# Kernel optimization log

Measured on AMD Instinct MI355X. Metric: run time of the kernel, lower is better.

## Reference

```python
import jax, jax.numpy as jnp
import numpy as np

N_VERTS = 40962   # icosphere level-6 vertices
N_POOL = 10242    # icosphere level-5 vertices (post-pool)
K = 7             # 6 neighbors + self
C1, C2, C3 = 64, 64, 128
IN_CH, OUT_CH = 8, 64
BATCH = 8


def setup_inputs() -> dict:
    key = jax.random.key(0)
    ks = jax.random.split(key, 10)
    x = jax.random.normal(ks[0], (BATCH, IN_CH, N_VERTS), dtype=jnp.float32)
    # neighbor order: 6 random neighbors + self at every 7th slot (as in my_get_neighs_order)
    neb6 = jax.random.randint(ks[1], (N_VERTS, 6), 0, N_VERTS)
    nebs = jnp.concatenate([neb6, jnp.arange(N_VERTS)[:, None]], axis=1).reshape(-1).astype(jnp.int64)
    s1 = 1.0 / np.sqrt(IN_CH)
    s2 = 1.0 / np.sqrt(C1 * K)
    s3 = 1.0 / np.sqrt(C2)
    sf = 1.0 / np.sqrt(C3 * N_POOL)
    W1 = jax.random.uniform(ks[2], (C1, IN_CH), jnp.float32, -s1, s1)
    b1 = jax.random.uniform(ks[3], (C1,), jnp.float32, -s1, s1)
    W2 = jax.random.uniform(ks[4], (C2, C1, K), jnp.float32, -s2, s2)
    b2 = jax.random.uniform(ks[5], (C2,), jnp.float32, -s2, s2)
    W3 = jax.random.uniform(ks[6], (C3, C2), jnp.float32, -s3, s3)
    b3 = jax.random.uniform(ks[7], (C3,), jnp.float32, -s3, s3)
    Wfc = jax.random.uniform(ks[8], (OUT_CH, C3 * N_POOL), jnp.float32, -sf, sf)
    bfc = jax.random.uniform(ks[9], (OUT_CH,), jnp.float32, -sf, sf)
    return {"x": x, "nebs": nebs, "W1": W1, "b1": b1, "W2": W2, "b2": b2,
            "W3": W3, "b3": b3, "Wfc": Wfc, "bfc": bfc}


def reference(x, nebs, W1, b1, W2, b2, W3, b3, Wfc, bfc):
    B = x.shape[0]
    # conv1: 1x1 conv == pointwise matmul over channels
    h1 = jax.nn.relu(jnp.einsum('bci,oc->boi', x, W1) + b1[None, :, None])  # [B,64,N]
    # gather neighbor features, then stride-7 conv collapses the 7 neighbor slots
    g1 = h1[:, :, nebs].reshape(B, C1, N_VERTS, K)                           # [B,64,N,7]
    h2 = jax.nn.relu(jnp.einsum('bcnk,ock->bon', g1, W2) + b2[None, :, None])  # [B,64,N]
    # gather for the first 10242 vertices, maxpool over the 7 neighbor slots
    g2 = h2[:, :, nebs[:N_POOL * K]].reshape(B, C2, N_POOL, K)
    p = jnp.max(g2, axis=-1)                                                  # [B,64,10242]
    # conv3: 1x1 conv
    h3 = jax.nn.relu(jnp.einsum('bci,oc->boi', p, W3) + b3[None, :, None])   # [B,128,10242]
    # dropout is identity in eval mode
    flat = h3.reshape(B, -1)                                                  # [B, 128*10242]
    return flat @ Wfc.T + bfc                                                 # [B, out_ch]
```

## Files before the change

### kernel.cpp

```cpp
#include <hip/hip_runtime.h>

#define NV 40962
#define NP 10242
#define KNB 7
#define C1 64
#define C2 64
#define C3 128
#define INC 8
#define OC 64
#define B 8
#define FCK (C3*NP)
#define NCHUNK (FCK/128)
#define FBLK 1024

typedef __attribute__((ext_vector_type(8))) __bf16 bf16x8;
typedef __attribute__((ext_vector_type(4))) float f32x4;
typedef unsigned short ushort_t;
typedef unsigned int uint_t;

static __device__ __forceinline__ ushort_t f2bf(float f) {
    uint_t u = __float_as_uint(f);
    u = (u + 0x7FFFu + ((u >> 16) & 1u)) >> 16;
    return (ushort_t)u;
}
static __device__ __forceinline__ uint_t pack2(float a, float b) {
    return (uint_t)f2bf(a) | ((uint_t)f2bf(b) << 16);
}

__global__ __launch_bounds__(256) void k_wswz(const float* __restrict__ W2,
        const float* __restrict__ W3, ushort_t* __restrict__ wsw) {
    int idx = blockIdx.x*256 + threadIdx.x;
    if (idx < 28672) {
        int j = idx & 7, lane = (idx >> 3) & 63, rest = idx >> 9;
        int ntile = rest & 3, kstep = rest >> 2;
        int quad = lane >> 4, col = lane & 15;
        int k = kstep*32 + quad*8 + j;
        int o = ntile*16 + col;
        int c = k & 63, knb = k >> 6;
        wsw[idx] = f2bf(W2[(size_t)o*(C1*KNB) + c*KNB + knb]);
    } else if (idx < 28672 + 8192) {
        int s = idx - 28672;
        int j = s & 7, lane = (s >> 3) & 63, rest = s >> 9;
        int ntile = rest & 7, kstep = rest >> 3;
        int quad = lane >> 4, col = lane & 15;
        int c = kstep*32 + quad*8 + j;
        int o3 = ntile*16 + col;
        wsw[idx] = f2bf(W3[(size_t)o3*C2 + c]);
    }
}

__global__ __launch_bounds__(256) void k_conv1(const float* __restrict__ x,
        const float* __restrict__ W1, const float* __restrict__ b1,
        ushort_t* __restrict__ h1bf) {
    __shared__ float sW[C1*INC];
    __shared__ float sb[C1];
    int tid = threadIdx.x;
    for (int i = tid; i < C1*INC; i += 256) sW[i] = W1[i];
    if (tid < C1) sb[tid] = b1[tid];
    __syncthreads();
    long g = (long)blockIdx.x*256 + tid;
    if (g >= (long)NV*B) return;
    int n = (int)(g >> 3);
    int b = (int)(g & 7);
    float xv[INC];
#pragma unroll
    for (int c = 0; c < INC; ++c) xv[c] = x[(size_t)b*INC*NV + (size_t)c*NV + n];
    uint4* outp = (uint4*)(h1bf + ((size_t)n*B + b)*C1);
#pragma unroll
    for (int og = 0; og < 8; ++og) {
        float h[8];
#pragma unroll
        for (int j = 0; j < 8; ++j) {
            int o = og*8 + j;
            float a = sb[o];
#pragma unroll
            for (int c = 0; c < INC; ++c) a += xv[c]*sW[o*INC + c];
            h[j] = fmaxf(a, 0.f);
        }
        uint4 u;
        u.x = pack2(h[0], h[1]); u.y = pack2(h[2], h[3]);
        u.z = pack2(h[4], h[5]); u.w = pack2(h[6], h[7]);
        outp[og] = u;
    }
}

__global__ __launch_bounds__(256) void k_conv2m(const ushort_t* __restrict__ h1bf,
        const int* __restrict__ nebs, const ushort_t* __restrict__ wsw,
        const float* __restrict__ b2, ushort_t* __restrict__ h2bf) {
    int tid = threadIdx.x;
    int wave = tid >> 6, lane = tid & 63;
    int quad = lane >> 4, col = lane & 15;
    int bsub = col & 7;
    int mblock = blockIdx.x * 128;
    int mbase[2];
    int rowt[2][KNB];
    f32x4 acc[2][4];
#pragma unroll
    for (int t = 0; t < 2; ++t) {
        mbase[t] = mblock + wave*32 + t*16;
        int v = (mbase[t] + col) >> 3;
        int vc = v < NV ? v : 0;
#pragma unroll
        for (int kn = 0; kn < KNB; ++kn) rowt[t][kn] = nebs[(size_t)vc*KNB + kn];
#pragma unroll
        for (int nt = 0; nt < 4; ++nt) acc[t][nt] = (f32x4){0.f, 0.f, 0.f, 0.f};
    }
    float bv[4];
#pragma unroll
    for (int nt = 0; nt < 4; ++nt) bv[nt] = b2[nt*16 + col];
    const bf16x8* W = (const bf16x8*)wsw;
#pragma unroll
    for (int ks = 0; ks < 14; ++ks) {
        int knb = ks >> 1;
        int c0 = (ks & 1)*32 + quad*8;
        bf16x8 a0 = *(const bf16x8*)(h1bf + ((size_t)rowt[0][knb]*B + bsub)*C1 + c0);
        bf16x8 a1 = *(const bf16x8*)(h1bf + ((size_t)rowt[1][knb]*B + bsub)*C1 + c0);
#pragma unroll
        for (int nt = 0; nt < 4; ++nt) {
            bf16x8 bf = W[(ks*4 + nt)*64 + lane];
            acc[0][nt] = __builtin_amdgcn_mfma_f32_16x16x32_bf16(a0, bf, acc[0][nt], 0, 0, 0);
            acc[1][nt] = __builtin_amdgcn_mfma_f32_16x16x32_bf16(a1, bf, acc[1][nt], 0, 0, 0);
        }
    }
#pragma unroll
    for (int t = 0; t < 2; ++t) {
#pragma unroll
        for (int r = 0; r < 4; ++r) {
            int m = mbase[t] + quad*4 + r;
            if ((m >> 3) < NV) {
#pragma unroll
                for (int nt = 0; nt < 4; ++nt) {
                    float val = fmaxf(acc[t][nt][r] + bv[nt], 0.f);
                    h2bf[(size_t)m*C2 + nt*16 + col] = f2bf(val);
                }
            }
        }
    }
}

__global__ __launch_bounds__(256) void k_pool(const ushort_t* __restrict__ h2bf,
        const int* __restrict__ nebs, ushort_t* __restrict__ pbf) {
    long t = (long)blockIdx.x*256 + threadIdx.x;
    if (t >= (long)NP*32) return;
    int cg = (int)(t & 3);
    int b  = (int)((t >> 2) & 7);
    int v  = (int)(t >> 5);
    float m[16];
#pragma unroll
    for (int i = 0; i < 16; ++i) m[i] = -1e30f;
    for (int kn = 0; kn < KNB; ++kn) {
        int row = nebs[(size_t)v*KNB + kn];
        const uint4* src = (const uint4*)(h2bf + ((size_t)row*B + b)*C2 + cg*16);
        uint4 u0 = src[0], u1 = src[1];
        uint_t ws[8] = {u0.x, u0.y, u0.z, u0.w, u1.x, u1.y, u1.z, u1.w};
#pragma unroll
        for (int i = 0; i < 8; ++i) {
            float lo = __uint_as_float((ws[i] & 0xFFFFu) << 16);
            float hi = __uint_as_float(ws[i] & 0xFFFF0000u);
            m[2*i]   = fmaxf(m[2*i], lo);
            m[2*i+1] = fmaxf(m[2*i+1], hi);
        }
    }
    uint_t op[8];
#pragma unroll
    for (int i = 0; i < 8; ++i) {
        uint_t lo = __float_as_uint(m[2*i]) >> 16;
        uint_t hi = __float_as_uint(m[2*i+1]) & 0xFFFF0000u;
        op[i] = lo | hi;
    }
    uint4* dst = (uint4*)(pbf + ((size_t)v*B + b)*C2 + cg*16);
    dst[0] = make_uint4(op[0], op[1], op[2], op[3]);
    dst[1] = make_uint4(op[4], op[5], op[6], op[7]);
}

__global__ __launch_bounds__(256) void k_conv3m(const ushort_t* __restrict__ pbf,
        const ushort_t* __restrict__ wsw3, const float* __restrict__ b3,
        float* __restrict__ h3) {
    int tid = threadIdx.x;
    int wave = tid >> 6, lane = tid & 63;
    int quad = lane >> 4, col = lane & 15;
    int m0 = blockIdx.x*64 + wave*16;
    int m = m0 + col;
    int mc = ((m >> 3) < NP) ? m : 0;
    f32x4 acc[8];
#pragma unroll
    for (int nt = 0; nt < 8; ++nt) acc[nt] = (f32x4){0.f, 0.f, 0.f, 0.f};
    float bv[8];
#pragma unroll
    for (int nt = 0; nt < 8; ++nt) bv[nt] = b3[nt*16 + col];
    const bf16x8* W = (const bf16x8*)wsw3;
#pragma unroll
    for (int ks = 0; ks < 2; ++ks) {
        bf16x8 a = *(const bf16x8*)(pbf + (size_t)mc*C2 + ks*32 + quad*8);
#pragma unroll
        for (int nt = 0; nt < 8; ++nt) {
            bf16x8 bf = W[(ks*8 + nt)*64 + lane];
            acc[nt] = __builtin_amdgcn_mfma_f32_16x16x32_bf16(a, bf, acc[nt], 0, 0, 0);
        }
    }
#pragma unroll
    for (int r = 0; r < 4; ++r) {
        int mm = m0 + quad*4 + r;
        int v = mm >> 3, b = mm & 7;
        if (v < NP) {
#pragma unroll
            for (int nt = 0; nt < 8; ++nt) {
                int o3 = nt*16 + col;
                h3[(size_t)b*FCK + (size_t)o3*NP + v] = fmaxf(acc[nt][r] + bv[nt], 0.f);
            }
        }
    }
}

__global__ __launch_bounds__(256) void k_fc(const float* __restrict__ h3,
        const float* __restrict__ Wfc, float* __restrict__ partial) {
    __shared__ float sH[B][128];
    __shared__ float sW[OC][129];
    int tid = threadIdx.x;
    int o = tid & 63;
    int tb = tid >> 6;
    float acc0 = 0.f, acc1 = 0.f;
    for (int ch = blockIdx.x; ch < NCHUNK; ch += FBLK) {
        size_t i0 = (size_t)ch * 128;
        __syncthreads();
        {
            int bb = tid >> 5, i4 = tid & 31;
            float4 f = *(const float4*)(h3 + (size_t)bb*FCK + i0 + i4*4);
            sH[bb][i4*4+0] = f.x; sH[bb][i4*4+1] = f.y;
            sH[bb][i4*4+2] = f.z; sH[bb][i4*4+3] = f.w;
        }
#pragma unroll
        for (int j = 0; j < 8; ++j) {
            int idx = tid + j*256;
            int oo = idx >> 5, i4 = idx & 31;
            float4 f = *(const float4*)(Wfc + (size_t)oo*FCK + i0 + i4*4);
            sW[oo][i4*4+0] = f.x; sW[oo][i4*4+1] = f.y;
            sW[oo][i4*4+2] = f.z; sW[oo][i4*4+3] = f.w;
        }
        __syncthreads();
#pragma unroll 8
        for (int ii = 0; ii < 128; ++ii) {
            float w = sW[o][ii];
            acc0 += w * sH[2*tb][ii];
            acc1 += w * sH[2*tb+1][ii];
        }
    }
    partial[((size_t)blockIdx.x*B + 2*tb  )*OC + o] = acc0;
    partial[((size_t)blockIdx.x*B + 2*tb+1)*OC + o] = acc1;
}

__global__ __launch_bounds__(256) void k_fcred(const float* __restrict__ partial,
        const float* __restrict__ bfc, float* __restrict__ out) {
    __shared__ float red[4][64];
    int b = blockIdx.x;
    int o = threadIdx.x & 63, jg = threadIdx.x >> 6;
    float s = 0.f;
    for (int j = jg; j < FBLK; j += 4) s += partial[((size_t)j*B + b)*OC + o];
    red[jg][o] = s;
    __syncthreads();
    if (jg == 0) out[b*OC + o] = red[0][o] + red[1][o] + red[2][o] + red[3][o] + bfc[o];
}

extern "C" void kernel_launch(void* const* d_in, const int* in_sizes, int n_in,
                              void* d_out, int out_size, void* d_ws, size_t ws_size,
                              hipStream_t stream) {
    const float* x    = (const float*)d_in[0];
    const int*   nebs = (const int*)d_in[1];
    const float* W1   = (const float*)d_in[2];
    const float* b1   = (const float*)d_in[3];
    const float* W2   = (const float*)d_in[4];
    const float* b2   = (const float*)d_in[5];
    const float* W3   = (const float*)d_in[6];
    const float* b3   = (const float*)d_in[7];
    const float* Wfc  = (const float*)d_in[8];
    const float* bfc  = (const float*)d_in[9];
    float* out = (float*)d_out;

    char* ws = (char*)d_ws;
    ushort_t* h1bf = (ushort_t*)(ws);
    ushort_t* h2bf = (ushort_t*)(ws + 42000000);
    ushort_t* pbf  = (ushort_t*)(ws + 84000000);
    float*    h3   = (float*)(ws + 96000000);
    ushort_t* wsw  = (ushort_t*)(ws + 140000000);
    float*    part = (float*)(ws + 141000000);
    ushort_t* wsw3 = wsw + 28672;

    k_wswz<<<144, 256, 0, stream>>>(W2, W3, wsw);
    k_conv1<<<1281, 256, 0, stream>>>(x, W1, b1, h1bf);
    k_conv2m<<<2561, 256, 0, stream>>>(h1bf, nebs, wsw, b2, h2bf);
    k_pool<<<1281, 256, 0, stream>>>(h2bf, nebs, pbf);
    k_conv3m<<<1281, 256, 0, stream>>>(pbf, wsw3, b3, h3);
    k_fc<<<FBLK, 256, 0, stream>>>(h3, Wfc, part);
    k_fcred<<<B, 256, 0, stream>>>(part, bfc, out);
}
```

Baseline: 670.3 us.

## Load FC weights directly into registers and split K across thread groups

The FC kernel no longer stages the large Wfc tile in shared memory. Each thread now loads a 2-output by 16-element weight slice into registers, reuses it across all 8 batch rows read from a small shared activation tile, and the eight K-slices are combined through a shared-memory reduction at the end. This removes the shared-memory round trip and most LDS reads for the weight stream, which dominates this memory-bound GEMV. The costs are more registers per thread and an extra reduction step per block.

```diff
diff --git a/kernel.cpp b/kernel.cpp
--- a/kernel.cpp
+++ b/kernel.cpp
@@ -215,38 +215,56 @@
 __global__ __launch_bounds__(256) void k_fc(const float* __restrict__ h3,
         const float* __restrict__ Wfc, float* __restrict__ partial) {
     __shared__ float sH[B][128];
-    __shared__ float sW[OC][129];
+    __shared__ float red[8][OC][8];
     int tid = threadIdx.x;
-    int o = tid & 63;
-    int tb = tid >> 6;
-    float acc0 = 0.f, acc1 = 0.f;
+    int og = tid & 31;
+    int ks = tid >> 5;
+    int o0 = og*2;
+    float acc[2][8];
+#pragma unroll
+    for (int r = 0; r < 2; ++r)
+#pragma unroll
+        for (int b = 0; b < 8; ++b) acc[r][b] = 0.f;
     for (int ch = blockIdx.x; ch < NCHUNK; ch += FBLK) {
         size_t i0 = (size_t)ch * 128;
         __syncthreads();
         {
             int bb = tid >> 5, i4 = tid & 31;
-            float4 f = *(const float4*)(h3 + (size_t)bb*FCK + i0 + i4*4);
-            sH[bb][i4*4+0] = f.x; sH[bb][i4*4+1] = f.y;
-            sH[bb][i4*4+2] = f.z; sH[bb][i4*4+3] = f.w;
-        }
-#pragma unroll
-        for (int j = 0; j < 8; ++j) {
-            int idx = tid + j*256;
-            int oo = idx >> 5, i4 = idx & 31;
-            float4 f = *(const float4*)(Wfc + (size_t)oo*FCK + i0 + i4*4);
-            sW[oo][i4*4+0] = f.x; sW[oo][i4*4+1] = f.y;
-            sW[oo][i4*4+2] = f.z; sW[oo][i4*4+3] = f.w;
-        }
+            *(f32x4*)&sH[bb][i4*4] = *(const f32x4*)(h3 + (size_t)bb*FCK + i0 + i4*4);
+        }
+        f32x4 w[2][4];
+#pragma unroll
+        for (int r = 0; r < 2; ++r)
+#pragma unroll
+            for (int q = 0; q < 4; ++q)
+                w[r][q] = *(const f32x4*)(Wfc + (size_t)(o0+r)*FCK + i0 + ks*16 + q*4);
         __syncthreads();
-#pragma unroll 8
-        for (int ii = 0; ii < 128; ++ii) {
-            float w = sW[o][ii];
-            acc0 += w * sH[2*tb][ii];
-            acc1 += w * sH[2*tb+1][ii];
-        }
-    }
-    partial[((size_t)blockIdx.x*B + 2*tb  )*OC + o] = acc0;
-    partial[((size_t)blockIdx.x*B + 2*tb+1)*OC + o] = acc1;
+#pragma unroll
+        for (int b = 0; b < 8; ++b) {
+#pragma unroll
+            for (int q = 0; q < 4; ++q) {
+                f32x4 h = *(const f32x4*)&sH[b][ks*16 + q*4];
+#pragma unroll
+                for (int r = 0; r < 2; ++r)
+                    acc[r][b] += w[r][q].x*h.x + w[r][q].y*h.y + w[r][q].z*h.z + w[r][q].w*h.w;
+            }
+        }
+    }
+#pragma unroll
+    for (int r = 0; r < 2; ++r) {
+        *(f32x4*)&red[ks][o0+r][0] = (f32x4){acc[r][0], acc[r][1], acc[r][2], acc[r][3]};
+        *(f32x4*)&red[ks][o0+r][4] = (f32x4){acc[r][4], acc[r][5], acc[r][6], acc[r][7]};
+    }
+    __syncthreads();
+#pragma unroll
+    for (int i = 0; i < 2; ++i) {
+        int idx = tid*2 + i;
+        int o = idx >> 3, b = idx & 7;
+        float s = 0.f;
+#pragma unroll
+        for (int k = 0; k < 8; ++k) s += red[k][o][b];
+        partial[((size_t)blockIdx.x*B + b)*OC + o] = s;
+    }
 }
 
 __global__ __launch_bounds__(256) void k_fcred(const float* __restrict__ partial,
```

Measured after the change: 669.1 us. No clear change (-0.2%).

## Fuse conv3 into FC via shared-memory tile and merge weight prep into conv1

Applied to the files above, without the earlier changes.

Conv3 now writes its ReLU outputs for a 16-vertex tile into a skewed shared-memory buffer, and the same block immediately computes that tile's FC partial sums. This removes the 42MB h3 round trip through global memory. The weight-swizzle kernel is merged into the conv1 launch as extra blocks, saving one launch. Block indices are remapped across XCDs for locality, and Wfc is still streamed once. The costs are a large shared-memory footprint (64KB plus the reduction buffer), which limits occupancy, and a more complex tail path.

```diff
diff --git a/kernel.cpp b/kernel.cpp
--- a/kernel.cpp
+++ b/kernel.cpp
@@ -10,8 +10,7 @@
 #define OC 64
 #define B 8
 #define FCK (C3*NP)
-#define NCHUNK (FCK/128)
-#define FBLK 1024
+#define NBLK_FC 641
 
 typedef __attribute__((ext_vector_type(8))) __bf16 bf16x8;
 typedef __attribute__((ext_vector_type(4))) float f32x4;
@@ -27,34 +26,34 @@
     return (uint_t)f2bf(a) | ((uint_t)f2bf(b) << 16);
 }
 
-__global__ __launch_bounds__(256) void k_wswz(const float* __restrict__ W2,
+__global__ __launch_bounds__(256) void k_pre(const float* __restrict__ x,
+        const float* __restrict__ W1, const float* __restrict__ b1,
+        ushort_t* __restrict__ h1bf, const float* __restrict__ W2,
         const float* __restrict__ W3, ushort_t* __restrict__ wsw) {
-    int idx = blockIdx.x*256 + threadIdx.x;
-    if (idx < 28672) {
-        int j = idx & 7, lane = (idx >> 3) & 63, rest = idx >> 9;
-        int ntile = rest & 3, kstep = rest >> 2;
-        int quad = lane >> 4, col = lane & 15;
-        int k = kstep*32 + quad*8 + j;
-        int o = ntile*16 + col;
-        int c = k & 63, knb = k >> 6;
-        wsw[idx] = f2bf(W2[(size_t)o*(C1*KNB) + c*KNB + knb]);
-    } else if (idx < 28672 + 8192) {
-        int s = idx - 28672;
-        int j = s & 7, lane = (s >> 3) & 63, rest = s >> 9;
-        int ntile = rest & 7, kstep = rest >> 3;
-        int quad = lane >> 4, col = lane & 15;
-        int c = kstep*32 + quad*8 + j;
-        int o3 = ntile*16 + col;
-        wsw[idx] = f2bf(W3[(size_t)o3*C2 + c]);
-    }
-}
-
-__global__ __launch_bounds__(256) void k_conv1(const float* __restrict__ x,
-        const float* __restrict__ W1, const float* __restrict__ b1,
-        ushort_t* __restrict__ h1bf) {
     __shared__ float sW[C1*INC];
     __shared__ float sb[C1];
     int tid = threadIdx.x;
+    if (blockIdx.x >= 1281) {
+        int idx = (blockIdx.x - 1281)*256 + tid;
+        if (idx < 28672) {
+            int j = idx & 7, lane = (idx >> 3) & 63, rest = idx >> 9;
+            int ntile = rest & 3, kstep = rest >> 2;
+            int quad = lane >> 4, col = lane & 15;
+            int k = kstep*32 + quad*8 + j;
+            int o = ntile*16 + col;
+            int c = k & 63, knb = k >> 6;
+            wsw[idx] = f2bf(W2[(size_t)o*(C1*KNB) + c*KNB + knb]);
+        } else if (idx < 28672 + 8192) {
+            int s = idx - 28672;
+            int j = s & 7, lane = (s >> 3) & 63, rest = s >> 9;
+            int ntile = rest & 7, kstep = rest >> 3;
+            int quad = lane >> 4, col = lane & 15;
+            int c = kstep*32 + quad*8 + j;
+            int o3 = ntile*16 + col;
+            wsw[idx] = f2bf(W3[(size_t)o3*C2 + c]);
+        }
+        return;
+    }
     for (int i = tid; i < C1*INC; i += 256) sW[i] = W1[i];
     if (tid < C1) sb[tid] = b1[tid];
     __syncthreads();
@@ -173,13 +172,20 @@
     dst[1] = make_uint4(op[4], op[5], op[6], op[7]);
 }
 
-__global__ __launch_bounds__(256) void k_conv3m(const ushort_t* __restrict__ pbf,
+__global__ __launch_bounds__(512) void k_pc3fc(const ushort_t* __restrict__ pbf,
         const ushort_t* __restrict__ wsw3, const float* __restrict__ b3,
-        float* __restrict__ h3) {
+        const float* __restrict__ Wfc, float* __restrict__ partial) {
+    __shared__ float sH3[128*128];
+    __shared__ float red[8][OC][8];
     int tid = threadIdx.x;
+    int bid = blockIdx.x;
+    const int q = NBLK_FC/8, r = NBLK_FC%8;
+    int xcd = bid & 7, cidx = bid >> 3;
+    int blk = (xcd < r) ? (xcd*(q+1) + cidx) : (r*(q+1) + (xcd-r)*q + cidx);
+    int v0 = blk*16;
     int wave = tid >> 6, lane = tid & 63;
     int quad = lane >> 4, col = lane & 15;
-    int m0 = blockIdx.x*64 + wave*16;
+    int m0 = blk*128 + wave*16;
     int m = m0 + col;
     int mc = ((m >> 3) < NP) ? m : 0;
     f32x4 acc[8];
@@ -199,54 +205,64 @@
         }
     }
 #pragma unroll
-    for (int r = 0; r < 4; ++r) {
-        int mm = m0 + quad*4 + r;
-        int v = mm >> 3, b = mm & 7;
-        if (v < NP) {
-#pragma unroll
-            for (int nt = 0; nt < 8; ++nt) {
-                int o3 = nt*16 + col;
-                h3[(size_t)b*FCK + (size_t)o3*NP + v] = fmaxf(acc[nt][r] + bv[nt], 0.f);
+    for (int nt = 0; nt < 8; ++nt) {
+        int o3 = nt*16 + col;
+        int mlb = wave*16 + quad*4;
+        f32x4 vals;
+#pragma unroll
+        for (int r4 = 0; r4 < 4; ++r4) {
+            int mm = m0 + quad*4 + r4;
+            vals[r4] = ((mm >> 3) < NP) ? fmaxf(acc[nt][r4] + bv[nt], 0.f) : 0.f;
+        }
+        int off = (mlb + ((o3 & 31) << 2)) & 127;
+        *(f32x4*)&sH3[o3*128 + off] = vals;
+    }
+    __syncthreads();
+    int o = tid & 63, ksl = tid >> 6;
+    float fa[8];
+#pragma unroll
+    for (int b = 0; b < 8; ++b) fa[b] = 0.f;
+    const float* wrow = Wfc + (size_t)o*FCK + v0;
+    if (v0 + 16 <= NP) {
+        for (int j = 0; j < 16; ++j) {
+            int o3 = ksl*16 + j;
+            float wv[16];
+            __builtin_memcpy(wv, wrow + (size_t)o3*NP, 64);
+            const float* hrow = &sH3[o3*128];
+            int skew = (o3 & 31) << 2;
+#pragma unroll
+            for (int vl = 0; vl < 16; ++vl) {
+                int base = (vl*8 + skew) & 127;
+                f32x4 h0 = *(const f32x4*)&hrow[base];
+                f32x4 h1 = *(const f32x4*)&hrow[(base + 4) & 127];
+                float w = wv[vl];
+                fa[0] += w*h0.x; fa[1] += w*h0.y; fa[2] += w*h0.z; fa[3] += w*h0.w;
+                fa[4] += w*h1.x; fa[5] += w*h1.y; fa[6] += w*h1.z; fa[7] += w*h1.w;
             }
         }
-    }
-}
-
-__global__ __launch_bounds__(256) void k_fc(const float* __restrict__ h3,
-        const float* __restrict__ Wfc, float* __restrict__ partial) {
-    __shared__ float sH[B][128];
-    __shared__ float sW[OC][129];
-    int tid = threadIdx.x;
-    int o = tid & 63;
-    int tb = tid >> 6;
-    float acc0 = 0.f, acc1 = 0.f;
-    for (int ch = blockIdx.x; ch < NCHUNK; ch += FBLK) {
-        size_t i0 = (size_t)ch * 128;
-        __syncthreads();
-        {
-            int bb = tid >> 5, i4 = tid & 31;
-            float4 f = *(const float4*)(h3 + (size_t)bb*FCK + i0 + i4*4);
-            sH[bb][i4*4+0] = f.x; sH[bb][i4*4+1] = f.y;
-            sH[bb][i4*4+2] = f.z; sH[bb][i4*4+3] = f.w;
-        }
-#pragma unroll
-        for (int j = 0; j < 8; ++j) {
-            int idx = tid + j*256;
-            int oo = idx >> 5, i4 = idx & 31;
-            float4 f = *(const float4*)(Wfc + (size_t)oo*FCK + i0 + i4*4);
-            sW[oo][i4*4+0] = f.x; sW[oo][i4*4+1] = f.y;
-            sW[oo][i4*4+2] = f.z; sW[oo][i4*4+3] = f.w;
-        }
-        __syncthreads();
-#pragma unroll 8
-        for (int ii = 0; ii < 128; ++ii) {
-            float w = sW[o][ii];
-            acc0 += w * sH[2*tb][ii];
-            acc1 += w * sH[2*tb+1][ii];
-        }
-    }
-    partial[((size_t)blockIdx.x*B + 2*tb  )*OC + o] = acc0;
-    partial[((size_t)blockIdx.x*B + 2*tb+1)*OC + o] = acc1;
+    } else {
+        int nv = NP - v0;
+        for (int j = 0; j < 16; ++j) {
+            int o3 = ksl*16 + j;
+            const float* hrow = &sH3[o3*128];
+            int skew = (o3 & 31) << 2;
+            for (int vl = 0; vl < nv; ++vl) {
+                int base = (vl*8 + skew) & 127;
+                f32x4 h0 = *(const f32x4*)&hrow[base];
+                f32x4 h1 = *(const f32x4*)&hrow[(base + 4) & 127];
+                float w = wrow[(size_t)o3*NP + vl];
+                fa[0] += w*h0.x; fa[1] += w*h0.y; fa[2] += w*h0.z; fa[3] += w*h0.w;
+                fa[4] += w*h1.x; fa[5] += w*h1.y; fa[6] += w*h1.z; fa[7] += w*h1.w;
+            }
+        }
+    }
+    *(f32x4*)&red[ksl][o][0] = (f32x4){fa[0], fa[1], fa[2], fa[3]};
+    *(f32x4*)&red[ksl][o][4] = (f32x4){fa[4], fa[5], fa[6], fa[7]};
+    __syncthreads();
+    float s = 0.f;
+#pragma unroll
+    for (int k = 0; k < 8; ++k) s += red[k][o][ksl];
+    partial[((size_t)blk*B + ksl)*OC + o] = s;
 }
 
 __global__ __launch_bounds__(256) void k_fcred(const float* __restrict__ partial,
@@ -255,7 +271,7 @@
     int b = blockIdx.x;
     int o = threadIdx.x & 63, jg = threadIdx.x >> 6;
     float s = 0.f;
-    for (int j = jg; j < FBLK; j += 4) s += partial[((size_t)j*B + b)*OC + o];
+    for (int j = jg; j < NBLK_FC; j += 4) s += partial[((size_t)j*B + b)*OC + o];
     red[jg][o] = s;
     __syncthreads();
     if (jg == 0) out[b*OC + o] = red[0][o] + red[1][o] + red[2][o] + red[3][o] + bfc[o];
@@ -280,16 +296,13 @@
     ushort_t* h1bf = (ushort_t*)(ws);
     ushort_t* h2bf = (ushort_t*)(ws + 42000000);
     ushort_t* pbf  = (ushort_t*)(ws + 84000000);
-    float*    h3   = (float*)(ws + 96000000);
     ushort_t* wsw  = (ushort_t*)(ws + 140000000);
     float*    part = (float*)(ws + 141000000);
     ushort_t* wsw3 = wsw + 28672;
 
-    k_wswz<<<144, 256, 0, stream>>>(W2, W3, wsw);
-    k_conv1<<<1281, 256, 0, stream>>>(x, W1, b1, h1bf);
+    k_pre<<<1425, 256, 0, stream>>>(x, W1, b1, h1bf, W2, W3, wsw);
     k_conv2m<<<2561, 256, 0, stream>>>(h1bf, nebs, wsw, b2, h2bf);
     k_pool<<<1281, 256, 0, stream>>>(h2bf, nebs, pbf);
-    k_conv3m<<<1281, 256, 0, stream>>>(pbf, wsw3, b3, h3);
-    k_fc<<<FBLK, 256, 0, stream>>>(h3, Wfc, part);
+    k_pc3fc<<<NBLK_FC, 512, 0, stream>>>(pbf, wsw3, b3, Wfc, part);
     k_fcred<<<B, 256, 0, stream>>>(part, bfc, out);
 }
```

New measurement: 628.9 us. 6.2% less time.
